# Kernel optimization log

Hardware: AMD Instinct MI355X
Metric: run time of the kernel (lower is better)

Reference implementation:

```python
import jax, jax.numpy as jnp
import numpy as np

# ---- constants from the source module ----
N_SAMPLES = 2 ** 15          # exp.n_samples
N_FRAMES = 128
N_HARMONICS = 8
N_EVENTS = 8
FILT_SIZE = 16               # freq_domain_filter_size
N_NOTES = 128                # len(scale)
NYQ = 22050.0 / 2.0          # samplerate nyquist
MIN_F0 = 40.0 / NYQ
F0_SPAN = (3000.0 / NYQ) - MIN_F0
MIN_RES = 0.5
RES_SPAN = 1.0 - MIN_RES
B_EVENTS = 128               # batch(16) * n_events(8)

# packed layout (build_param_slices order):
SL_F0 = slice(0, N_NOTES)                       # 0:128
SL_AMP = slice(N_NOTES + N_FRAMES, N_NOTES + 2 * N_FRAMES)   # 256:384
SL_HAMP = slice(N_NOTES + 2 * N_FRAMES, N_NOTES + 2 * N_FRAMES + N_HARMONICS)  # 384:392
SL_HDEC = slice(N_NOTES + 2 * N_FRAMES + N_HARMONICS, N_NOTES + 2 * N_FRAMES + 2 * N_HARMONICS)  # 392:400
SL_FENV = slice(N_NOTES + 2 * N_FRAMES + 2 * N_HARMONICS, N_NOTES + 2 * N_FRAMES + 2 * N_HARMONICS + FILT_SIZE)  # 400:416


def interp_linear(x, out_size):
    """F.interpolate(..., mode='linear', align_corners=False) on last dim of [B,C,L]."""
    L = x.shape[-1]
    scale = L / out_size
    coords = (jnp.arange(out_size, dtype=x.dtype) + 0.5) * scale - 0.5
    coords = jnp.clip(coords, 0.0, L - 1)
    i0 = jnp.floor(coords).astype(jnp.int32)
    i1 = jnp.minimum(i0 + 1, L - 1)
    w = coords - i0.astype(x.dtype)
    return x[..., i0] * (1.0 - w) + x[..., i1] * w


def setup_inputs() -> dict:
    key = jax.random.key(0)
    k1, k2 = jax.random.split(key)
    packed = jax.random.uniform(k1, (B_EVENTS, N_NOTES + 2 * N_FRAMES + 2 * N_HARMONICS + FILT_SIZE), dtype=jnp.float32)
    # musical-scale center frequencies, normalized by nyquist (geometric 20..3000 Hz)
    hz = 20.0 * (3000.0 / 20.0) ** (np.arange(N_NOTES) / (N_NOTES - 1))
    frequencies = jnp.asarray(hz / NYQ, dtype=jnp.float32)
    global_amp = jnp.full((1,), 5000.0, dtype=jnp.float32)
    osc_amp = jnp.full((1,), 50.0, dtype=jnp.float32)
    noise = jax.random.uniform(k2, (B_EVENTS, 1, N_SAMPLES), dtype=jnp.float32, minval=-1.0, maxval=1.0)
    return {"packed": packed, "frequencies": frequencies, "global_amp": global_amp,
            "osc_amp": osc_amp, "noise": noise}


def reference(packed, frequencies, global_amp, osc_amp, noise):
    B = packed.shape[0]
    # ---- f0 (discrete): softmax over notes, expectation, squared, repeated per frame ----
    f0_scalar = jax.nn.softmax(packed[:, SL_F0], axis=-1) @ frequencies          # [B]
    f0 = (f0_scalar ** 2)[:, None, None] * jnp.ones((1, 1, N_FRAMES), packed.dtype)  # [B,1,F]
    f0 = f0 * NYQ
    f0 = MIN_F0 + f0 * F0_SPAN
    # (the torch line `f0 + f0 + f0_fine` has no assignment -> no effect; f0_fine unused)

    # ---- oscillator bank ----
    harm_factors = jnp.arange(1, N_HARMONICS + 1, dtype=packed.dtype)
    osc = f0 * harm_factors[None, :, None]                      # [B,H,F]
    radians = osc / NYQ * jnp.pi
    radians = jnp.where(radians >= jnp.pi, 0.0, radians)
    radians = interp_linear(radians, N_SAMPLES)                  # [B,H,S]
    osc_bank = jnp.sin(jnp.cumsum(radians, axis=-1)) * osc_amp   # [B,H,S]

    # ---- per-harmonic amplitude recurrence (scan over frames) ----
    harm_decay = MIN_RES + packed[:, SL_HDEC] * RES_SPAN         # [B,H]
    harm_amp = packed[:, SL_HAMP]                                # [B,H]
    amp = packed[:, SL_AMP][:, None, :] * 2.0 - 1.0              # [B,1,F]

    def step(current, amp_i):                                    # current [B,H], amp_i [B,1]
        cur = jnp.maximum(current + amp_i * harm_amp, 0.0)       # clamp(0, inf)
        return cur * harm_decay, cur

    amp_frames = jnp.moveaxis(amp[:, 0, :], 1, 0)[:, :, None]    # [F,B,1]
    _, res = jax.lax.scan(step, jnp.zeros((B, N_HARMONICS), packed.dtype), amp_frames)
    res = jnp.moveaxis(res, 0, 2)                                # [B,H,F]
    res_full = interp_linear(res, N_SAMPLES)                     # [B,H,S]

    # ---- FFT-filtered noise ----
    amp_full = interp_linear(amp, N_SAMPLES)                     # [B,1,S]
    nf = packed[:, SL_FENV][:, None, :]                          # [B,1,16]
    nf = interp_linear(nf, N_SAMPLES // 2)
    nf = jnp.pad(nf, ((0, 0), (0, 0), (0, 1)))                   # [B,1,S//2+1]
    noise_scaled = noise * global_amp
    spec = jnp.fft.rfft(noise_scaled, axis=-1, norm='ortho')
    filt = spec * nf
    noise_out = jnp.fft.irfft(filt, n=N_SAMPLES, axis=-1, norm='ortho')
    noise_out = noise_out * jnp.where(amp_full >= 0, amp_full, 0.2 * amp_full)  # leaky_relu(0.2)

    # ---- combine ----
    x = res_full * osc_bank                                      # [B,H,S]
    x = noise_out / N_HARMONICS + x                              # broadcast [B,1,S]
    x = x.reshape(-1, N_EVENTS, N_HARMONICS, N_SAMPLES)
    x = jnp.sum(x, axis=(1, 2)).reshape(-1, 1, N_SAMPLES)        # [batch,1,S]
    return x
```

## Files before the change

### kernel.cpp

```cpp
#include <hip/hip_runtime.h>
#include <math.h>

#define PCK_STRIDE 416
#define N_SAMPLES  32768
#define FFT_M      16384
#define HN         8192
#define B_EVENTS   128
#define N_GROUPS   16
#define NT         1024
#define PI_F 3.14159265358979323846f
#define RT2H 0.70710678118654752f

#define MAP(i) ((i) + (((i) >> 5) << 2))
#define LDS_H  9216

__device__ inline float filt_at(const float* __restrict__ f, int k) {
    if (k >= FFT_M) return 0.0f;
    float c = ((float)k + 0.5f) * (1.0f / 1024.0f) - 0.5f;
    c = fminf(fmaxf(c, 0.0f), 15.0f);
    int i0 = (int)floorf(c);
    int i1 = min(i0 + 1, 15);
    float w = c - (float)i0;
    return f[i0] * (1.0f - w) + f[i1] * w;
}

template<int L>
__device__ inline void r4_dif_stage(float* re, float* im, int tid) {
    constexpr int q = L >> 2;
    constexpr float ang = -6.28318530717958647692f / (float)L;
    #pragma unroll 1
    for (int s = 0; s < (HN / 4) / NT; ++s) {
        int m = tid + s * NT;
        int t = m & (q - 1);
        int i0 = ((m & ~(q - 1)) << 2) | t;
        int ia = MAP(i0), ib = MAP(i0 + q), ic = MAP(i0 + 2 * q), id = MAP(i0 + 3 * q);
        float ar = re[ia], ai = im[ia];
        float br = re[ib], bi = im[ib];
        float cr = re[ic], ci = im[ic];
        float dr = re[id], di = im[id];
        float s1, c1; __sincosf(ang * (float)t, &s1, &c1);
        float c2 = c1 * c1 - s1 * s1, s2 = 2.0f * c1 * s1;
        float c3 = c2 * c1 - s2 * s1, s3 = c2 * s1 + s2 * c1;
        float s0r = ar + cr, s0i = ai + ci;
        float t1r = br + dr, t1i = bi + di;
        float d0r = ar - cr, d0i = ai - ci;
        float d1r = br - dr, d1i = bi - di;
        re[ia] = s0r + t1r; im[ia] = s0i + t1i;
        float er = s0r - t1r, ei = s0i - t1i;
        re[ib] = er * c2 - ei * s2; im[ib] = er * s2 + ei * c2;
        float fr = d0r + d1i, fi = d0i - d1r;
        re[ic] = fr * c1 - fi * s1; im[ic] = fr * s1 + fi * c1;
        float gr = d0r - d1i, gi = d0i + d1r;
        re[id] = gr * c3 - gi * s3; im[id] = gr * s3 + gi * c3;
    }
    __syncthreads();
}

template<int L>
__device__ inline void r4_dit_stage(float* re, float* im, int tid) {
    constexpr int q = L >> 2;
    constexpr float ang = 6.28318530717958647692f / (float)L;
    #pragma unroll 1
    for (int s = 0; s < (HN / 4) / NT; ++s) {
        int m = tid + s * NT;
        int t = m & (q - 1);
        int i0 = ((m & ~(q - 1)) << 2) | t;
        int ia = MAP(i0), ib = MAP(i0 + q), ic = MAP(i0 + 2 * q), id = MAP(i0 + 3 * q);
        float ar = re[ia], ai = im[ia];
        float br = re[ib], bi = im[ib];
        float cr = re[ic], ci = im[ic];
        float dr = re[id], di = im[id];
        float s1, c1; __sincosf(ang * (float)t, &s1, &c1);
        float c2 = c1 * c1 - s1 * s1, s2 = 2.0f * c1 * s1;
        float tbr = br * c2 - bi * s2, tbi = br * s2 + bi * c2;
        float tdr = dr * c2 - di * s2, tdi = dr * s2 + di * c2;
        float B0r = ar + tbr, B0i = ai + tbi;
        float B1r = ar - tbr, B1i = ai - tbi;
        float B2r = cr + tdr, B2i = ci + tdi;
        float B3r = cr - tdr, B3i = ci - tdi;
        float t0r = B2r * c1 - B2i * s1, t0i = B2r * s1 + B2i * c1;
        float t1r = -B3r * s1 - B3i * c1, t1i = B3r * c1 - B3i * s1;
        re[ia] = B0r + t0r; im[ia] = B0i + t0i;
        re[ib] = B1r + t1r; im[ib] = B1i + t1i;
        re[ic] = B0r - t0r; im[ic] = B0i - t0i;
        re[id] = B1r - t1r; im[id] = B1i - t1i;
    }
    __syncthreads();
}

__global__ __launch_bounds__(NT)
void fft_half_kernel(
    const float* __restrict__ noise, const float* __restrict__ packed,
    const float* __restrict__ gamp, float2* __restrict__ hd,
    const float* __restrict__ freqs, float* __restrict__ rW, float* __restrict__ res)
{
    extern __shared__ float smem[];
    float* re = smem;
    float* im = smem + LDS_H;
    float* filt = smem + 2 * LDS_H;
    const int half = blockIdx.x;
    const int b = blockIdx.y;
    const int tid = threadIdx.x;
    const float g = gamp[0];

    const float2* nz = (const float2*)(noise + (size_t)b * N_SAMPLES);
    if (half == 0) {
        #pragma unroll 1
        for (int s = 0; s < HN / NT; ++s) {
            int j = tid + s * NT;
            float2 v0 = nz[j];
            float2 v1 = nz[j + HN];
            float ur = v0.x * g, ui = v0.y * g;
            float wr = v1.x * g, wi = v1.y * g;
            int a0 = MAP(j);
            re[a0] = ur + wr; im[a0] = ui + wi;
        }
    } else {
        #pragma unroll 1
        for (int s = 0; s < HN / NT; ++s) {
            int j = tid + s * NT;
            float2 v0 = nz[j];
            float2 v1 = nz[j + HN];
            float ur = v0.x * g, ui = v0.y * g;
            float wr = v1.x * g, wi = v1.y * g;
            float dr = ur - wr, di = ui - wi;
            float s1, c1; __sincosf((-PI_F / 8192.0f) * (float)j, &s1, &c1);
            int a0 = MAP(j);
            re[a0] = dr * c1 - di * s1;
            im[a0] = dr * s1 + di * c1;
        }
    }
    if (tid >= 64 && tid < 80) filt[tid - 64] = packed[b * PCK_STRIDE + 400 + (tid - 64)];

    if (half == 0 && tid < 64) {
        const float* row = packed + b * PCK_STRIDE;
        float n0 = row[tid], n1 = row[tid + 64];
        float fq0 = freqs[tid], fq1 = freqs[tid + 64];
        float mx = fmaxf(n0, n1);
        #pragma unroll
        for (int off = 32; off >= 1; off >>= 1) mx = fmaxf(mx, __shfl_xor(mx, off));
        float e0 = __expf(n0 - mx), e1 = __expf(n1 - mx);
        float den = e0 + e1, num = e0 * fq0 + e1 * fq1;
        #pragma unroll
        for (int off = 32; off >= 1; off >>= 1) {
            den += __shfl_xor(den, off);
            num += __shfl_xor(num, off);
        }
        float ampA = row[256 + tid] * 2.0f - 1.0f;
        float ampB = row[320 + tid] * 2.0f - 1.0f;
        int h = tid & 7;
        float ha = row[384 + h];
        float hdcy = 0.5f + row[392 + h] * 0.5f;
        const float MIN_F0 = 40.0f / 11025.0f;
        const float F0_SPAN = 3000.0f / 11025.0f - 40.0f / 11025.0f;
        float f0s = num / den;
        float f0 = MIN_F0 + f0s * f0s * 11025.0f * F0_SPAN;
        float r = f0 * (float)(h + 1) * (PI_F / 11025.0f);
        if (r >= PI_F) r = 0.0f;
        if (tid < 8) rW[b * 8 + tid] = r;
        float cur = 0.0f;
        float* rr = res + (b * 8 + h) * 128;
        for (int f = 0; f < 64; ++f) {
            float av = __shfl(ampA, f);
            float c = fmaxf(cur + av * ha, 0.0f);
            if (tid < 8) rr[f] = c;
            cur = c * hdcy;
        }
        for (int f = 0; f < 64; ++f) {
            float av = __shfl(ampB, f);
            float c = fmaxf(cur + av * ha, 0.0f);
            if (tid < 8) rr[64 + f] = c;
            cur = c * hdcy;
        }
    }
    __syncthreads();

    r4_dif_stage<8192>(re, im, tid);
    r4_dif_stage<2048>(re, im, tid);
    r4_dif_stage<512>(re, im, tid);
    r4_dif_stage<128>(re, im, tid);
    r4_dif_stage<32>(re, im, tid);

    #pragma unroll 1
    for (int s = 0; s < (HN / 8) / NT; ++s) {
        int m = ((HN / 8) / NT) * tid + s;
        int a = MAP(8 * m);
        float4 r0 = *(const float4*)(re + a);
        float4 r1 = *(const float4*)(re + a + 4);
        float4 q0 = *(const float4*)(im + a);
        float4 q1 = *(const float4*)(im + a + 4);
        float t0r = r0.x + r1.x, t0i = q0.x + q1.x;
        float u0r = r0.x - r1.x, u0i = q0.x - q1.x;
        float d1r = r0.y - r1.y, d1i = q0.y - q1.y;
        float t1r = r0.y + r1.y, t1i = q0.y + q1.y;
        float u1r = RT2H * (d1r + d1i), u1i = RT2H * (d1i - d1r);
        float t2r = r0.z + r1.z, t2i = q0.z + q1.z;
        float d2r = r0.z - r1.z, d2i = q0.z - q1.z;
        float u2r = d2i, u2i = -d2r;
        float t3r = r0.w + r1.w, t3i = q0.w + q1.w;
        float d3r = r0.w - r1.w, d3i = q0.w - q1.w;
        float u3r = RT2H * (d3i - d3r), u3i = -RT2H * (d3r + d3i);
        float A0r = t0r + t2r, A0i = t0i + t2i;
        float A2r = t0r - t2r, A2i = t0i - t2i;
        float A1r = t1r + t3r, A1i = t1i + t3i;
        float e3r = t1r - t3r, e3i = t1i - t3i;
        float A3r = e3i, A3i = -e3r;
        float B0r = u0r + u2r, B0i = u0i + u2i;
        float B2r = u0r - u2r, B2i = u0i - u2i;
        float B1r = u1r + u3r, B1i = u1i + u3i;
        float f3r = u1r - u3r, f3i = u1i - u3i;
        float B3r = f3i, B3i = -f3r;
        r0.x = A0r + A1r; q0.x = A0i + A1i;
        r0.y = A0r - A1r; q0.y = A0i - A1i;
        r0.z = A2r + A3r; q0.z = A2i + A3i;
        r0.w = A2r - A3r; q0.w = A2i - A3i;
        r1.x = B0r + B1r; q1.x = B0i + B1i;
        r1.y = B0r - B1r; q1.y = B0i - B1i;
        r1.z = B2r + B3r; q1.z = B2i + B3i;
        r1.w = B2r - B3r; q1.w = B2i - B3i;
        *(float4*)(re + a) = r0; *(float4*)(re + a + 4) = r1;
        *(float4*)(im + a) = q0; *(float4*)(im + a + 4) = q1;
    }
    __syncthreads();

    const float invM = 1.0f / (float)FFT_M;
    #pragma unroll 1
    for (int s = 0; s < (HN / 2) / NT; ++s) {
        int p = (tid + s * NT) << 1;
        int jj = (half << 13) | p;
        if (jj == 0) {
            int p0 = MAP(0);
            float z0r = re[p0], z0i = im[p0];
            float y = 0.5f * filt_at(filt, 0) * (z0r + z0i) * invM;
            re[p0] = y; im[p0] = y;
            int p1 = MAP(1);
            float H = filt_at(filt, 8192) * invM;
            re[p1] *= H; im[p1] *= H;
        } else {
            int k = (int)(__brev((unsigned)jj) >> 18);
            int kq = FFT_M - k;
            int pk = MAP(p);
            int pq = MAP((int)(__brev((unsigned)kq) >> 18) & (HN - 1));
            float zkr = re[pk], zki = im[pk];
            float zqr = re[pq], zqi = im[pq];
            float Er = 0.5f * (zkr + zqr), Ei = 0.5f * (zki - zqi);
            float Or = 0.5f * (zki + zqi), Oi = 0.5f * (zqr - zkr);
            float th = (float)k * (PI_F / (float)FFT_M);
            float s1, c1; __sincosf(th, &s1, &c1);
            float ts = -s1;
            float tOr = c1 * Or - ts * Oi;
            float tOi = c1 * Oi + ts * Or;
            float Hk = filt_at(filt, k);
            float Hq = filt_at(filt, kq);
            float Ykr = Hk * (Er + tOr), Yki = Hk * (Ei + tOi);
            float Cr  = Hq * (Er - tOr), Ci  = Hq * (Ei - tOi);
            float Ar = 0.5f * (Ykr + Cr), Ai = 0.5f * (Yki + Ci);
            float Br = 0.5f * (Ykr - Cr), Bi = 0.5f * (Yki - Ci);
            re[pk] = (Ar + ts * Br - c1 * Bi) * invM;
            im[pk] = (Ai + c1 * Br + ts * Bi) * invM;
            re[pq] = (Ar + c1 * Bi - ts * Br) * invM;
            im[pq] = (-Ai + c1 * Br + ts * Bi) * invM;
        }
    }
    __syncthreads();

    #pragma unroll 1
    for (int s = 0; s < (HN / 8) / NT; ++s) {
        int m = ((HN / 8) / NT) * tid + s;
        int a = MAP(8 * m);
        float4 r0 = *(const float4*)(re + a);
        float4 r1 = *(const float4*)(re + a + 4);
        float4 q0 = *(const float4*)(im + a);
        float4 q1 = *(const float4*)(im + a + 4);
        float A0r = r0.x + r0.y, A0i = q0.x + q0.y;
        float A1r = r0.x - r0.y, A1i = q0.x - q0.y;
        float A2r = r0.z + r0.w, A2i = q0.z + q0.w;
        float A3r = r0.z - r0.w, A3i = q0.z - q0.w;
        float B0r = r1.x + r1.y, B0i = q1.x + q1.y;
        float B1r = r1.x - r1.y, B1i = q1.x - q1.y;
        float B2r = r1.z + r1.w, B2i = q1.z + q1.w;
        float B3r = r1.z - r1.w, B3i = q1.z - q1.w;
        float t0r = A0r + A2r, t0i = A0i + A2i;
        float t2r = A0r - A2r, t2i = A0i - A2i;
        float w3r = -A3i, w3i = A3r;
        float t1r = A1r + w3r, t1i = A1i + w3i;
        float t3r = A1r - w3r, t3i = A1i - w3i;
        float u0r = B0r + B2r, u0i = B0i + B2i;
        float u2r = B0r - B2r, u2i = B0i - B2i;
        float x3r = -B3i, x3i = B3r;
        float u1r = B1r + x3r, u1i = B1i + x3i;
        float u3r = B1r - x3r, u3i = B1i - x3i;
        float w1r = RT2H * (u1r - u1i), w1i = RT2H * (u1r + u1i);
        float w2r = -u2i,               w2i = u2r;
        float w5r = RT2H * (-u3r - u3i), w5i = RT2H * (u3r - u3i);
        r0.x = t0r + u0r; q0.x = t0i + u0i;
        r1.x = t0r - u0r; q1.x = t0i - u0i;
        r0.y = t1r + w1r; q0.y = t1i + w1i;
        r1.y = t1r - w1r; q1.y = t1i - w1i;
        r0.z = t2r + w2r; q0.z = t2i + w2i;
        r1.z = t2r - w2r; q1.z = t2i - w2i;
        r0.w = t3r + w5r; q0.w = t3i + w5i;
        r1.w = t3r - w5r; q1.w = t3i - w5i;
        *(float4*)(re + a) = r0; *(float4*)(re + a + 4) = r1;
        *(float4*)(im + a) = q0; *(float4*)(im + a + 4) = q1;
    }
    __syncthreads();

    r4_dit_stage<32>(re, im, tid);
    r4_dit_stage<128>(re, im, tid);
    r4_dit_stage<512>(re, im, tid);
    r4_dit_stage<2048>(re, im, tid);
    r4_dit_stage<8192>(re, im, tid);

    float2* dst = hd + (size_t)b * FFT_M + (half << 13);
    #pragma unroll 1
    for (int s = 0; s < HN / NT; ++s) {
        int j = tid + s * NT;
        dst[j] = make_float2(re[MAP(j)], im[MAP(j)]);
    }
}

__global__ __launch_bounds__(256) void assemble_kernel(
    const float* __restrict__ packed, const float* __restrict__ rW,
    const float* __restrict__ res, const float2* __restrict__ hd,
    const float* __restrict__ oamp, float* __restrict__ out)
{
    const int g = blockIdx.y;
    const int chunk = blockIdx.x;
    const int tid = threadIdx.x;
    const int n = chunk * 256 + tid;
    const int fb = chunk - 1;

    __shared__ float s_res[8][8][3];
    __shared__ float s_ampf[8][3];
    __shared__ float s_r[8][8];
    if (tid < 192) {
        int e = tid / 24, rem = tid % 24, h = rem / 3, j = rem % 3;
        int f = min(max(fb + j, 0), 127);
        s_res[e][h][j] = res[((g * 8 + e) * 8 + h) * 128 + f];
    }
    if (tid < 24) {
        int e = tid / 3, j = tid % 3;
        int f = min(max(fb + j, 0), 127);
        s_ampf[e][j] = packed[(g * 8 + e) * PCK_STRIDE + 256 + f] * 2.0f - 1.0f;
    }
    if (tid >= 192 && tid < 256) {
        int u = tid - 192;
        s_r[u / 8][u % 8] = rW[g * 64 + u];
    }
    __syncthreads();

    float coords = ((float)n + 0.5f) * (1.0f / 256.0f) - 0.5f;
    coords = fminf(fmaxf(coords, 0.0f), 127.0f);
    int i0 = (int)floorf(coords);
    float w = coords - (float)i0;
    int j0 = i0 - fb;
    float osc50 = oamp[0];
    float pn = (float)(n + 1);
    float wm = 1.0f - w;

    const int jglob = n >> 1;
    const int jl = jglob & (HN - 1);
    const bool lo = (jglob < HN);
    float sx, cx; __sincosf((PI_F / 8192.0f) * (float)jl, &sx, &cx);

    float acc = 0.0f;
    #pragma unroll
    for (int e = 0; e < 8; ++e) {
        int b = g * 8 + e;
        const float2* hb = hd + (size_t)b * FFT_M;
        float2 U = hb[jl];
        float2 X = hb[jl + HN];
        float wr2 = X.x * cx - X.y * sx;
        float wi2 = X.x * sx + X.y * cx;
        float nr = lo ? (U.x + wr2) : (U.x - wr2);
        float ni = lo ? (U.y + wi2) : (U.y - wi2);
        float nv = (n & 1) ? ni : nr;
        float av = s_ampf[e][j0] * wm + s_ampf[e][j0 + 1] * w;
        float gate = (av >= 0.0f) ? av : 0.2f * av;
        acc += nv * gate;
        float sn, cn; __sincosf(pn * s_r[e][0], &sn, &cn);
        float c2 = 2.0f * cn;
        float shm1 = 0.0f, sh = sn;
        #pragma unroll
        for (int h = 0; h < 8; ++h) {
            float rsv = s_res[e][h][j0] * wm + s_res[e][h][j0 + 1] * w;
            float sv = (s_r[e][h] != 0.0f) ? sh : 0.0f;
            acc += rsv * osc50 * sv;
            float nx = c2 * sh - shm1;
            shm1 = sh; sh = nx;
        }
    }
    out[(size_t)g * N_SAMPLES + n] = acc;
}

extern "C" void kernel_launch(void* const* d_in, const int* in_sizes, int n_in,
                              void* d_out, int out_size, void* d_ws, size_t ws_size,
                              hipStream_t stream) {
    const float* packed = (const float*)d_in[0];
    const float* freqs  = (const float*)d_in[1];
    const float* gamp   = (const float*)d_in[2];
    const float* oamp   = (const float*)d_in[3];
    const float* noise  = (const float*)d_in[4];
    float* out = (float*)d_out;

    float* ws = (float*)d_ws;
    float2* hd = (float2*)ws;
    float* res = ws + (size_t)B_EVENTS * N_SAMPLES;
    float* rW  = res + B_EVENTS * 8 * 128;

    fft_half_kernel<<<dim3(2, B_EVENTS), NT, (2 * LDS_H + 16) * sizeof(float), stream>>>(
        noise, packed, gamp, hd, freqs, rW, res);
    assemble_kernel<<<dim3(N_SAMPLES / 256, N_GROUPS), 256, 0, stream>>>(
        packed, rW, res, hd, oamp, out);
}
```

Measured before the change: 107.2 us.

## Interleave FFT data as complex float2 in LDS and compute two samples per assemble thread

The FFT kernel now keeps interleaved complex float2 values in shared memory instead of separate real and imaginary arrays, so each butterfly does one 64-bit LDS access per point rather than two 32-bit ones. The assemble kernel has each thread produce two adjacent output samples. Both samples come from the same complex spectrum value, which removes the duplicate global loads of the U/X pairs and the duplicated twiddle work per event. The grid is halved and the output is written as float2. The risks are LDS bank conflicts from the wider strided float2 accesses under the existing padding map, and higher register pressure in the assemble loop.

```diff
diff --git a/kernel.cpp b/kernel.cpp
--- a/kernel.cpp
+++ b/kernel.cpp
@@ -25,7 +25,7 @@
 }
 
 template<int L>
-__device__ inline void r4_dif_stage(float* re, float* im, int tid) {
+__device__ inline void r4_dif_stage(float2* z, int tid) {
     constexpr int q = L >> 2;
     constexpr float ang = -6.28318530717958647692f / (float)L;
     #pragma unroll 1
@@ -34,30 +34,27 @@
         int t = m & (q - 1);
         int i0 = ((m & ~(q - 1)) << 2) | t;
         int ia = MAP(i0), ib = MAP(i0 + q), ic = MAP(i0 + 2 * q), id = MAP(i0 + 3 * q);
-        float ar = re[ia], ai = im[ia];
-        float br = re[ib], bi = im[ib];
-        float cr = re[ic], ci = im[ic];
-        float dr = re[id], di = im[id];
+        float2 A = z[ia], B = z[ib], C = z[ic], D = z[id];
         float s1, c1; __sincosf(ang * (float)t, &s1, &c1);
         float c2 = c1 * c1 - s1 * s1, s2 = 2.0f * c1 * s1;
         float c3 = c2 * c1 - s2 * s1, s3 = c2 * s1 + s2 * c1;
-        float s0r = ar + cr, s0i = ai + ci;
-        float t1r = br + dr, t1i = bi + di;
-        float d0r = ar - cr, d0i = ai - ci;
-        float d1r = br - dr, d1i = bi - di;
-        re[ia] = s0r + t1r; im[ia] = s0i + t1i;
+        float s0r = A.x + C.x, s0i = A.y + C.y;
+        float t1r = B.x + D.x, t1i = B.y + D.y;
+        float d0r = A.x - C.x, d0i = A.y - C.y;
+        float d1r = B.x - D.x, d1i = B.y - D.y;
+        z[ia] = make_float2(s0r + t1r, s0i + t1i);
         float er = s0r - t1r, ei = s0i - t1i;
-        re[ib] = er * c2 - ei * s2; im[ib] = er * s2 + ei * c2;
+        z[ib] = make_float2(er * c2 - ei * s2, er * s2 + ei * c2);
         float fr = d0r + d1i, fi = d0i - d1r;
-        re[ic] = fr * c1 - fi * s1; im[ic] = fr * s1 + fi * c1;
+        z[ic] = make_float2(fr * c1 - fi * s1, fr * s1 + fi * c1);
         float gr = d0r - d1i, gi = d0i + d1r;
-        re[id] = gr * c3 - gi * s3; im[id] = gr * s3 + gi * c3;
+        z[id] = make_float2(gr * c3 - gi * s3, gr * s3 + gi * c3);
     }
     __syncthreads();
 }
 
 template<int L>
-__device__ inline void r4_dit_stage(float* re, float* im, int tid) {
+__device__ inline void r4_dit_stage(float2* z, int tid) {
     constexpr int q = L >> 2;
     constexpr float ang = 6.28318530717958647692f / (float)L;
     #pragma unroll 1
@@ -66,24 +63,21 @@
         int t = m & (q - 1);
         int i0 = ((m & ~(q - 1)) << 2) | t;
         int ia = MAP(i0), ib = MAP(i0 + q), ic = MAP(i0 + 2 * q), id = MAP(i0 + 3 * q);
-        float ar = re[ia], ai = im[ia];
-        float br = re[ib], bi = im[ib];
-        float cr = re[ic], ci = im[ic];
-        float dr = re[id], di = im[id];
+        float2 A = z[ia], B = z[ib], C = z[ic], D = z[id];
         float s1, c1; __sincosf(ang * (float)t, &s1, &c1);
         float c2 = c1 * c1 - s1 * s1, s2 = 2.0f * c1 * s1;
-        float tbr = br * c2 - bi * s2, tbi = br * s2 + bi * c2;
-        float tdr = dr * c2 - di * s2, tdi = dr * s2 + di * c2;
-        float B0r = ar + tbr, B0i = ai + tbi;
-        float B1r = ar - tbr, B1i = ai - tbi;
-        float B2r = cr + tdr, B2i = ci + tdi;
-        float B3r = cr - tdr, B3i = ci - tdi;
+        float tbr = B.x * c2 - B.y * s2, tbi = B.x * s2 + B.y * c2;
+        float tdr = D.x * c2 - D.y * s2, tdi = D.x * s2 + D.y * c2;
+        float B0r = A.x + tbr, B0i = A.y + tbi;
+        float B1r = A.x - tbr, B1i = A.y - tbi;
+        float B2r = C.x + tdr, B2i = C.y + tdi;
+        float B3r = C.x - tdr, B3i = C.y - tdi;
         float t0r = B2r * c1 - B2i * s1, t0i = B2r * s1 + B2i * c1;
         float t1r = -B3r * s1 - B3i * c1, t1i = B3r * c1 - B3i * s1;
-        re[ia] = B0r + t0r; im[ia] = B0i + t0i;
-        re[ib] = B1r + t1r; im[ib] = B1i + t1i;
-        re[ic] = B0r - t0r; im[ic] = B0i - t0i;
-        re[id] = B1r - t1r; im[id] = B1i - t1i;
+        z[ia] = make_float2(B0r + t0r, B0i + t0i);
+        z[ib] = make_float2(B1r + t1r, B1i + t1i);
+        z[ic] = make_float2(B0r - t0r, B0i - t0i);
+        z[id] = make_float2(B1r - t1r, B1i - t1i);
     }
     __syncthreads();
 }
@@ -95,8 +89,7 @@
     const float* __restrict__ freqs, float* __restrict__ rW, float* __restrict__ res)
 {
     extern __shared__ float smem[];
-    float* re = smem;
-    float* im = smem + LDS_H;
+    float2* z = (float2*)smem;
     float* filt = smem + 2 * LDS_H;
     const int half = blockIdx.x;
     const int b = blockIdx.y;
@@ -110,10 +103,7 @@
             int j = tid + s * NT;
             float2 v0 = nz[j];
             float2 v1 = nz[j + HN];
-            float ur = v0.x * g, ui = v0.y * g;
-            float wr = v1.x * g, wi = v1.y * g;
-            int a0 = MAP(j);
-            re[a0] = ur + wr; im[a0] = ui + wi;
+            z[MAP(j)] = make_float2((v0.x + v1.x) * g, (v0.y + v1.y) * g);
         }
     } else {
         #pragma unroll 1
@@ -121,13 +111,9 @@
             int j = tid + s * NT;
             float2 v0 = nz[j];
             float2 v1 = nz[j + HN];
-            float ur = v0.x * g, ui = v0.y * g;
-            float wr = v1.x * g, wi = v1.y * g;
-            float dr = ur - wr, di = ui - wi;
+            float dr = (v0.x - v1.x) * g, di = (v0.y - v1.y) * g;
             float s1, c1; __sincosf((-PI_F / 8192.0f) * (float)j, &s1, &c1);
-            int a0 = MAP(j);
-            re[a0] = dr * c1 - di * s1;
-            im[a0] = dr * s1 + di * c1;
+            z[MAP(j)] = make_float2(dr * c1 - di * s1, dr * s1 + di * c1);
         }
     }
     if (tid >= 64 && tid < 80) filt[tid - 64] = packed[b * PCK_STRIDE + 400 + (tid - 64)];
@@ -175,30 +161,30 @@
     }
     __syncthreads();
 
-    r4_dif_stage<8192>(re, im, tid);
-    r4_dif_stage<2048>(re, im, tid);
-    r4_dif_stage<512>(re, im, tid);
-    r4_dif_stage<128>(re, im, tid);
-    r4_dif_stage<32>(re, im, tid);
+    r4_dif_stage<8192>(z, tid);
+    r4_dif_stage<2048>(z, tid);
+    r4_dif_stage<512>(z, tid);
+    r4_dif_stage<128>(z, tid);
+    r4_dif_stage<32>(z, tid);
 
     #pragma unroll 1
     for (int s = 0; s < (HN / 8) / NT; ++s) {
         int m = ((HN / 8) / NT) * tid + s;
-        int a = MAP(8 * m);
-        float4 r0 = *(const float4*)(re + a);
-        float4 r1 = *(const float4*)(re + a + 4);
-        float4 q0 = *(const float4*)(im + a);
-        float4 q1 = *(const float4*)(im + a + 4);
-        float t0r = r0.x + r1.x, t0i = q0.x + q1.x;
-        float u0r = r0.x - r1.x, u0i = q0.x - q1.x;
-        float d1r = r0.y - r1.y, d1i = q0.y - q1.y;
-        float t1r = r0.y + r1.y, t1i = q0.y + q1.y;
+        float* base = (float*)(z + MAP(8 * m));
+        float4 f0 = *(const float4*)(base);
+        float4 f1 = *(const float4*)(base + 4);
+        float4 f2 = *(const float4*)(base + 8);
+        float4 f3 = *(const float4*)(base + 12);
+        float t0r = f0.x + f2.x, t0i = f0.y + f2.y;
+        float u0r = f0.x - f2.x, u0i = f0.y - f2.y;
+        float t1r = f0.z + f2.z, t1i = f0.w + f2.w;
+        float d1r = f0.z - f2.z, d1i = f0.w - f2.w;
         float u1r = RT2H * (d1r + d1i), u1i = RT2H * (d1i - d1r);
-        float t2r = r0.z + r1.z, t2i = q0.z + q1.z;
-        float d2r = r0.z - r1.z, d2i = q0.z - q1.z;
+        float t2r = f1.x + f3.x, t2i = f1.y + f3.y;
+        float d2r = f1.x - f3.x, d2i = f1.y - f3.y;
         float u2r = d2i, u2i = -d2r;
-        float t3r = r0.w + r1.w, t3i = q0.w + q1.w;
-        float d3r = r0.w - r1.w, d3i = q0.w - q1.w;
+        float t3r = f1.z + f3.z, t3i = f1.w + f3.w;
+        float d3r = f1.z - f3.z, d3i = f1.w - f3.w;
         float u3r = RT2H * (d3i - d3r), u3i = -RT2H * (d3r + d3i);
         float A0r = t0r + t2r, A0i = t0i + t2i;
         float A2r = t0r - t2r, A2i = t0i - t2i;
@@ -210,16 +196,12 @@
         float B1r = u1r + u3r, B1i = u1i + u3i;
         float f3r = u1r - u3r, f3i = u1i - u3i;
         float B3r = f3i, B3i = -f3r;
-        r0.x = A0r + A1r; q0.x = A0i + A1i;
-        r0.y = A0r - A1r; q0.y = A0i - A1i;
-        r0.z = A2r + A3r; q0.z = A2i + A3i;
-        r0.w = A2r - A3r; q0.w = A2i - A3i;
-        r1.x = B0r + B1r; q1.x = B0i + B1i;
-        r1.y = B0r - B1r; q1.y = B0i - B1i;
-        r1.z = B2r + B3r; q1.z = B2i + B3i;
-        r1.w = B2r - B3r; q1.w = B2i - B3i;
-        *(float4*)(re + a) = r0; *(float4*)(re + a + 4) = r1;
-        *(float4*)(im + a) = q0; *(float4*)(im + a + 4) = q1;
+        f0.x = A0r + A1r; f0.y = A0i + A1i; f0.z = A0r - A1r; f0.w = A0i - A1i;
+        f1.x = A2r + A3r; f1.y = A2i + A3i; f1.z = A2r - A3r; f1.w = A2i - A3i;
+        f2.x = B0r + B1r; f2.y = B0i + B1i; f2.z = B0r - B1r; f2.w = B0i - B1i;
+        f3.x = B2r + B3r; f3.y = B2i + B3i; f3.z = B2r - B3r; f3.w = B2i - B3i;
+        *(float4*)(base) = f0; *(float4*)(base + 4) = f1;
+        *(float4*)(base + 8) = f2; *(float4*)(base + 12) = f3;
     }
     __syncthreads();
 
@@ -229,22 +211,21 @@
         int p = (tid + s * NT) << 1;
         int jj = (half << 13) | p;
         if (jj == 0) {
-            int p0 = MAP(0);
-            float z0r = re[p0], z0i = im[p0];
-            float y = 0.5f * filt_at(filt, 0) * (z0r + z0i) * invM;
-            re[p0] = y; im[p0] = y;
-            int p1 = MAP(1);
+            float2 z0 = z[MAP(0)];
+            float y = 0.5f * filt_at(filt, 0) * (z0.x + z0.y) * invM;
+            z[MAP(0)] = make_float2(y, y);
             float H = filt_at(filt, 8192) * invM;
-            re[p1] *= H; im[p1] *= H;
+            float2 z1 = z[MAP(1)];
+            z[MAP(1)] = make_float2(z1.x * H, z1.y * H);
         } else {
             int k = (int)(__brev((unsigned)jj) >> 18);
             int kq = FFT_M - k;
             int pk = MAP(p);
             int pq = MAP((int)(__brev((unsigned)kq) >> 18) & (HN - 1));
-            float zkr = re[pk], zki = im[pk];
-            float zqr = re[pq], zqi = im[pq];
-            float Er = 0.5f * (zkr + zqr), Ei = 0.5f * (zki - zqi);
-            float Or = 0.5f * (zki + zqi), Oi = 0.5f * (zqr - zkr);
+            float2 zk = z[pk];
+            float2 zq = z[pq];
+            float Er = 0.5f * (zk.x + zq.x), Ei = 0.5f * (zk.y - zq.y);
+            float Or = 0.5f * (zk.y + zq.y), Oi = 0.5f * (zq.x - zk.x);
             float th = (float)k * (PI_F / (float)FFT_M);
             float s1, c1; __sincosf(th, &s1, &c1);
             float ts = -s1;
@@ -256,10 +237,10 @@
             float Cr  = Hq * (Er - tOr), Ci  = Hq * (Ei - tOi);
             float Ar = 0.5f * (Ykr + Cr), Ai = 0.5f * (Yki + Ci);
             float Br = 0.5f * (Ykr - Cr), Bi = 0.5f * (Yki - Ci);
-            re[pk] = (Ar + ts * Br - c1 * Bi) * invM;
-            im[pk] = (Ai + c1 * Br + ts * Bi) * invM;
-            re[pq] = (Ar + c1 * Bi - ts * Br) * invM;
-            im[pq] = (-Ai + c1 * Br + ts * Bi) * invM;
+            z[pk] = make_float2((Ar + ts * Br - c1 * Bi) * invM,
+                                (Ai + c1 * Br + ts * Bi) * invM);
+            z[pq] = make_float2((Ar + c1 * Bi - ts * Br) * invM,
+                                (-Ai + c1 * Br + ts * Bi) * invM);
         }
     }
     __syncthreads();
@@ -267,19 +248,19 @@
     #pragma unroll 1
     for (int s = 0; s < (HN / 8) / NT; ++s) {
         int m = ((HN / 8) / NT) * tid + s;
-        int a = MAP(8 * m);
-        float4 r0 = *(const float4*)(re + a);
-        float4 r1 = *(const float4*)(re + a + 4);
-        float4 q0 = *(const float4*)(im + a);
-        float4 q1 = *(const float4*)(im + a + 4);
-        float A0r = r0.x + r0.y, A0i = q0.x + q0.y;
-        float A1r = r0.x - r0.y, A1i = q0.x - q0.y;
-        float A2r = r0.z + r0.w, A2i = q0.z + q0.w;
-        float A3r = r0.z - r0.w, A3i = q0.z - q0.w;
-        float B0r = r1.x + r1.y, B0i = q1.x + q1.y;
-        float B1r = r1.x - r1.y, B1i = q1.x - q1.y;
-        float B2r = r1.z + r1.w, B2i = q1.z + q1.w;
-        float B3r = r1.z - r1.w, B3i = q1.z - q1.w;
+        float* base = (float*)(z + MAP(8 * m));
+        float4 f0 = *(const float4*)(base);
+        float4 f1 = *(const float4*)(base + 4);
+        float4 f2 = *(const float4*)(base + 8);
+        float4 f3 = *(const float4*)(base + 12);
+        float A0r = f0.x + f0.z, A0i = f0.y + f0.w;
+        float A1r = f0.x - f0.z, A1i = f0.y - f0.w;
+        float A2r = f1.x + f1.z, A2i = f1.y + f1.w;
+        float A3r = f1.x - f1.z, A3i = f1.y - f1.w;
+        float B0r = f2.x + f2.z, B0i = f2.y + f2.w;
+        float B1r = f2.x - f2.z, B1i = f2.y - f2.w;
+        float B2r = f3.x + f3.z, B2i = f3.y + f3.w;
+        float B3r = f3.x - f3.z, B3i = f3.y - f3.w;
         float t0r = A0r + A2r, t0i = A0i + A2i;
         float t2r = A0r - A2r, t2i = A0i - A2i;
         float w3r = -A3i, w3i = A3r;
@@ -293,30 +274,30 @@
         float w1r = RT2H * (u1r - u1i), w1i = RT2H * (u1r + u1i);
         float w2r = -u2i,               w2i = u2r;
         float w5r = RT2H * (-u3r - u3i), w5i = RT2H * (u3r - u3i);
-        r0.x = t0r + u0r; q0.x = t0i + u0i;
-        r1.x = t0r - u0r; q1.x = t0i - u0i;
-        r0.y = t1r + w1r; q0.y = t1i + w1i;
-        r1.y = t1r - w1r; q1.y = t1i - w1i;
-        r0.z = t2r + w2r; q0.z = t2i + w2i;
-        r1.z = t2r - w2r; q1.z = t2i - w2i;
-        r0.w = t3r + w5r; q0.w = t3i + w5i;
-        r1.w = t3r - w5r; q1.w = t3i - w5i;
-        *(float4*)(re + a) = r0; *(float4*)(re + a + 4) = r1;
-        *(float4*)(im + a) = q0; *(float4*)(im + a + 4) = q1;
-    }
-    __syncthreads();
-
-    r4_dit_stage<32>(re, im, tid);
-    r4_dit_stage<128>(re, im, tid);
-    r4_dit_stage<512>(re, im, tid);
-    r4_dit_stage<2048>(re, im, tid);
-    r4_dit_stage<8192>(re, im, tid);
+        f0.x = t0r + u0r; f0.y = t0i + u0i;
+        f0.z = t1r + w1r; f0.w = t1i + w1i;
+        f1.x = t2r + w2r; f1.y = t2i + w2i;
+        f1.z = t3r + w5r; f1.w = t3i + w5i;
+        f2.x = t0r - u0r; f2.y = t0i - u0i;
+        f2.z = t1r - w1r; f2.w = t1i - w1i;
+        f3.x = t2r - w2r; f3.y = t2i - w2i;
+        f3.z = t3r - w5r; f3.w = t3i - w5i;
+        *(float4*)(base) = f0; *(float4*)(base + 4) = f1;
+        *(float4*)(base + 8) = f2; *(float4*)(base + 12) = f3;
+    }
+    __syncthreads();
+
+    r4_dit_stage<32>(z, tid);
+    r4_dit_stage<128>(z, tid);
+    r4_dit_stage<512>(z, tid);
+    r4_dit_stage<2048>(z, tid);
+    r4_dit_stage<8192>(z, tid);
 
     float2* dst = hd + (size_t)b * FFT_M + (half << 13);
     #pragma unroll 1
     for (int s = 0; s < HN / NT; ++s) {
         int j = tid + s * NT;
-        dst[j] = make_float2(re[MAP(j)], im[MAP(j)]);
+        dst[j] = z[MAP(j)];
     }
 }
 
@@ -328,43 +309,40 @@
     const int g = blockIdx.y;
     const int chunk = blockIdx.x;
     const int tid = threadIdx.x;
-    const int n = chunk * 256 + tid;
-    const int fb = chunk - 1;
-
-    __shared__ float s_res[8][8][3];
-    __shared__ float s_ampf[8][3];
+    const int n0 = chunk * 512 + 2 * tid;
+    const int fb = 2 * chunk - 1;
+
+    __shared__ float s_res[8][8][4];
+    __shared__ float s_ampf[8][4];
     __shared__ float s_r[8][8];
-    if (tid < 192) {
-        int e = tid / 24, rem = tid % 24, h = rem / 3, j = rem % 3;
+    {
+        int e = tid >> 5, rem = tid & 31, h = rem >> 2, j = rem & 3;
         int f = min(max(fb + j, 0), 127);
         s_res[e][h][j] = res[((g * 8 + e) * 8 + h) * 128 + f];
     }
-    if (tid < 24) {
-        int e = tid / 3, j = tid % 3;
+    if (tid < 32) {
+        int e = tid >> 2, j = tid & 3;
         int f = min(max(fb + j, 0), 127);
         s_ampf[e][j] = packed[(g * 8 + e) * PCK_STRIDE + 256 + f] * 2.0f - 1.0f;
-    }
-    if (tid >= 192 && tid < 256) {
-        int u = tid - 192;
-        s_r[u / 8][u % 8] = rW[g * 64 + u];
-    }
-    __syncthreads();
-
-    float coords = ((float)n + 0.5f) * (1.0f / 256.0f) - 0.5f;
-    coords = fminf(fmaxf(coords, 0.0f), 127.0f);
-    int i0 = (int)floorf(coords);
-    float w = coords - (float)i0;
-    int j0 = i0 - fb;
+    } else if (tid < 96) {
+        int u = tid - 32;
+        s_r[u >> 3][u & 7] = rW[g * 64 + u];
+    }
+    __syncthreads();
+
+    float c0 = fminf(fmaxf(((float)n0 + 0.5f) * (1.0f / 256.0f) - 0.5f, 0.0f), 127.0f);
+    float c1v = fminf(fmaxf(((float)n0 + 1.5f) * (1.0f / 256.0f) - 0.5f, 0.0f), 127.0f);
+    int i00 = (int)floorf(c0);  float w0 = c0 - (float)i00;  int ja = i00 - fb;
+    int i01 = (int)floorf(c1v); float w1 = c1v - (float)i01; int jb = i01 - fb;
+    float wm0 = 1.0f - w0, wm1 = 1.0f - w1;
     float osc50 = oamp[0];
-    float pn = (float)(n + 1);
-    float wm = 1.0f - w;
-
-    const int jglob = n >> 1;
-    const int jl = jglob & (HN - 1);
-    const bool lo = (jglob < HN);
+    float pn0 = (float)(n0 + 1), pn1 = (float)(n0 + 2);
+
+    const int jl = ((chunk & 31) << 8) | tid;
+    const bool lo = (chunk < 32);
     float sx, cx; __sincosf((PI_F / 8192.0f) * (float)jl, &sx, &cx);
 
-    float acc = 0.0f;
+    float acc0 = 0.0f, acc1 = 0.0f;
     #pragma unroll
     for (int e = 0; e < 8; ++e) {
         int b = g * 8 + e;
@@ -375,23 +353,28 @@
         float wi2 = X.x * sx + X.y * cx;
         float nr = lo ? (U.x + wr2) : (U.x - wr2);
         float ni = lo ? (U.y + wi2) : (U.y - wi2);
-        float nv = (n & 1) ? ni : nr;
-        float av = s_ampf[e][j0] * wm + s_ampf[e][j0 + 1] * w;
-        float gate = (av >= 0.0f) ? av : 0.2f * av;
-        acc += nv * gate;
-        float sn, cn; __sincosf(pn * s_r[e][0], &sn, &cn);
-        float c2 = 2.0f * cn;
-        float shm1 = 0.0f, sh = sn;
+        float av0 = s_ampf[e][ja] * wm0 + s_ampf[e][ja + 1] * w0;
+        float av1 = s_ampf[e][jb] * wm1 + s_ampf[e][jb + 1] * w1;
+        acc0 += nr * ((av0 >= 0.0f) ? av0 : 0.2f * av0);
+        acc1 += ni * ((av1 >= 0.0f) ? av1 : 0.2f * av1);
+        float r1 = s_r[e][0];
+        float sn0, cn0; __sincosf(pn0 * r1, &sn0, &cn0);
+        float sn1, cn1; __sincosf(pn1 * r1, &sn1, &cn1);
+        float c20 = 2.0f * cn0, c21 = 2.0f * cn1;
+        float sm0 = 0.0f, sh0 = sn0;
+        float sm1 = 0.0f, sh1 = sn1;
         #pragma unroll
         for (int h = 0; h < 8; ++h) {
-            float rsv = s_res[e][h][j0] * wm + s_res[e][h][j0 + 1] * w;
-            float sv = (s_r[e][h] != 0.0f) ? sh : 0.0f;
-            acc += rsv * osc50 * sv;
-            float nx = c2 * sh - shm1;
-            shm1 = sh; sh = nx;
-        }
-    }
-    out[(size_t)g * N_SAMPLES + n] = acc;
+            float rs0 = s_res[e][h][ja] * wm0 + s_res[e][h][ja + 1] * w0;
+            float rs1 = s_res[e][h][jb] * wm1 + s_res[e][h][jb + 1] * w1;
+            bool nzr = (s_r[e][h] != 0.0f);
+            acc0 += rs0 * osc50 * (nzr ? sh0 : 0.0f);
+            acc1 += rs1 * osc50 * (nzr ? sh1 : 0.0f);
+            float nx0 = c20 * sh0 - sm0; sm0 = sh0; sh0 = nx0;
+            float nx1 = c21 * sh1 - sm1; sm1 = sh1; sh1 = nx1;
+        }
+    }
+    *(float2*)(out + (size_t)g * N_SAMPLES + n0) = make_float2(acc0, acc1);
 }
 
 extern "C" void kernel_launch(void* const* d_in, const int* in_sizes, int n_in,
@@ -411,6 +394,6 @@
 
     fft_half_kernel<<<dim3(2, B_EVENTS), NT, (2 * LDS_H + 16) * sizeof(float), stream>>>(
         noise, packed, gamp, hd, freqs, rW, res);
-    assemble_kernel<<<dim3(N_SAMPLES / 256, N_GROUPS), 256, 0, stream>>>(
+    assemble_kernel<<<dim3(N_SAMPLES / 512, N_GROUPS), 256, 0, stream>>>(
         packed, rW, res, hd, oamp, out);
 }
```

Measured after the change: 107.5 us. Within noise of the previous version (+0.3%).
